# Kernel optimization log

Hardware: AMD Instinct MI355X
Metric: run time of the kernel (lower is better)

## Reference

```python
import jax, jax.numpy as jnp
import numpy as np

EPS = 1e-8

def _unit(v):
    # matches unitization(): v / (||v|| + 1e-8), norm over last (xyz) axis
    return v / (jnp.linalg.norm(v, axis=-1, keepdims=True) + EPS)

def setup_inputs() -> dict:
    key = jax.random.key(0)
    ks = jax.random.split(key, 6)
    B, C, P, S = 16, 76, 1024, 32  # 12 + C_in(=64) channels
    inp = jax.random.normal(ks[0], (B, C, P, S), jnp.float32)
    normal = jax.random.normal(ks[1], (B, P, 3), jnp.float32)
    w1 = jax.random.normal(ks[2], (128, 73), jnp.float32) * 0.1
    b1 = jnp.zeros((128,), jnp.float32)
    w2 = jax.random.normal(ks[3], (128, 128), jnp.float32) * 0.1
    b2 = jnp.zeros((128,), jnp.float32)
    return {"input": inp, "normal": normal, "w1": w1, "b1": b1, "w2": w2, "b2": b2}

def reference(input, normal, w1, b1, w2, b2):
    # channel layout: [0:3]=abs coords, [3:6]=neighbor normals, [6:9]=relative coords,
    # [9:12]=neighbor azimuth dirs, [12:]=input features (C_in=64)
    other_normal = input[:, 3:6]   # (B,3,P,S)
    rel = input[:, 6:9]            # (B,3,P,S)
    other_dir = input[:, 9:12]     # (B,3,P,S)
    feats = input[:, 12:]          # (B,C_in,P,S)

    # azimuth vector: mean of relative coords over neighbors excluding centroid slot
    azi = jnp.mean(rel[:, :, :, 1:], axis=3).transpose(0, 2, 1)  # (B,P,3)

    # PointAlign rotation: local frame with z = unit normal,
    # x = azimuth projected onto tangent plane, y = z x x (row-stacked rotation)
    n = _unit(normal)
    a = _unit(azi)
    xax = _unit(a - jnp.sum(a * n, axis=-1, keepdims=True) * n)
    yax = jnp.cross(n, xax)
    R = jnp.stack([xax, yax, n], axis=2)  # (B,P,3,3)

    def align(v):  # (B,3,P,S) -> (B,3,P,S): rotate each neighbor vector into local frame
        return jnp.einsum('bpij,bjps->bips', R, v)

    azi_u = _unit(azi)                                  # (B,P,3)
    dir_dif = align(azi_u.transpose(0, 2, 1)[:, :, :, None] - other_dir)

    # x[:,0:3] = aligned relative coords, then concat other_normal + dir_difs
    x = jnp.concatenate([align(rel), feats, align(other_normal), dir_dif], axis=1)  # (B,73,P,S)

    # shared MLP: two 1x1 convs + ReLU
    h = jax.nn.relu(jnp.einsum('oc,bcps->bops', w1, x) + b1[None, :, None, None])
    h = jax.nn.relu(jnp.einsum('oc,bcps->bops', w2, h) + b2[None, :, None, None])

    pooled = jnp.max(h, axis=3)  # max_pool2d over nsample -> (B,128,P)
    # not last layer: prepend unit azimuth vector
    return jnp.concatenate([azi_u.transpose(0, 2, 1), pooled], axis=1)  # (B,131,P)
```

## Files before the change

### kernel.cpp

```cpp
#include <hip/hip_runtime.h>
#include <hip/hip_bf16.h>

#define NB 16
#define NP 1024
#define NS 32
#define NC 76
#define XSTR 104
#define HSTR 136
#define TPB 16

typedef __attribute__((ext_vector_type(8))) short bf16x8;
typedef __attribute__((ext_vector_type(4))) float f32x4;

__device__ inline short f2bf(float f) {
  unsigned u = __builtin_bit_cast(unsigned, f);
  u = u + 0x7fffu + ((u >> 16) & 1u);
  return (short)(u >> 16);
}
__device__ inline unsigned cvt_pk_bf16(float lo, float hi) {
  unsigned r;
  asm("v_cvt_pk_bf16_f32 %0, %1, %2" : "=v"(r) : "v"(lo), "v"(hi));
  return r;
}
__device__ inline int swzx(int col, int k) {
  return (col * XSTR + k) ^ (((col >> 4) & 7) << 3);
}
__device__ inline int swzh(int col, int k) {
  return (col * HSTR + k) ^ (((col >> 4) & 7) << 3);
}
__device__ inline float dpp_max16(float v) {
  int x;
  x = __builtin_amdgcn_update_dpp(0, __builtin_bit_cast(int, v), 0xB1, 0xf, 0xf, true);
  v = fmaxf(v, __builtin_bit_cast(float, x));
  x = __builtin_amdgcn_update_dpp(0, __builtin_bit_cast(int, v), 0x4E, 0xf, 0xf, true);
  v = fmaxf(v, __builtin_bit_cast(float, x));
  x = __builtin_amdgcn_update_dpp(0, __builtin_bit_cast(int, v), 0x141, 0xf, 0xf, true);
  v = fmaxf(v, __builtin_bit_cast(float, x));
  x = __builtin_amdgcn_update_dpp(0, __builtin_bit_cast(int, v), 0x140, 0xf, 0xf, true);
  v = fmaxf(v, __builtin_bit_cast(float, x));
  return v;
}

__global__ __launch_bounds__(512, 2)
void mlp_kernel(const float* __restrict__ inp, const float* __restrict__ w1g,
                const float* __restrict__ b1g, const float* __restrict__ w2g,
                const float* __restrict__ b2g, const float* __restrict__ normal,
                float* __restrict__ out) {
  __shared__ short xb[2][128 * XSTR];
  __shared__ short hb[2][128 * HSTR];
  const int tid = threadIdx.x;
  const int lane = tid & 63;
  const int wv = tid >> 6;
  const int wr = wv >> 1;
  const int wc = wv & 1;
  const int l15 = lane & 15;
  const int l4 = lane >> 4;

  const int tile0 = blockIdx.x * TPB;

  const int s4  = tid & 7;
  const int flp = (tid >> 3) & 3;
  const int chq = tid >> 5;
  const int colb = flp*32 + 4*s4;

  bf16x8 w1f[2][3];
#pragma unroll
  for (int mf = 0; mf < 2; ++mf)
#pragma unroll
    for (int ks = 0; ks < 3; ++ks) {
      bf16x8 a;
#pragma unroll
      for (int j = 0; j < 8; ++j) {
        int row = 32*wr + 16*mf + l15;
        int kk = 32*ks + 8*l4 + j;
        float v = 0.f;
        if (kk < 73) {
          int c = (kk < 64) ? (kk + 3) : ((kk < 67) ? (kk - 64) : kk);
          v = w1g[row*73 + c];
        } else if (kk == 73) {
          v = b1g[row];
        }
        a[j] = f2bf(v);
      }
      w1f[mf][ks] = a;
    }
  bf16x8 w2f[2][4];
#pragma unroll
  for (int mf = 0; mf < 2; ++mf)
#pragma unroll
    for (int ks = 0; ks < 4; ++ks) {
      bf16x8 a;
#pragma unroll
      for (int j = 0; j < 8; ++j) {
        int row = 32*wr + 16*mf + l15;
        int kk = 32*ks + 8*l4 + j;
        a[j] = f2bf(w2g[row*128 + kk]);
      }
      w2f[mf][ks] = a;
    }
  float bias2[2][4];
#pragma unroll
  for (int mf = 0; mf < 2; ++mf)
#pragma unroll
    for (int r = 0; r < 4; ++r)
      bias2[mf][r] = b2g[32*wr + 16*mf + 4*l4 + r];

  for (int i = tid; i < 2*128*23; i += 512) {
    int bufi = i / (128*23);
    int r = i - bufi*(128*23);
    int col = r / 23;
    int k = 73 + (r - col*23);
    xb[bufi][swzx(col, k)] = (k == 73) ? (short)0x3F80 : (short)0;
  }

  float4 sf0, sf1, sf2, sf3;
  float sro[9];
  auto stage = [&](int it2) {
    const int tile = tile0 + it2;
    const int bb = tile >> 8;
    const int pb = (tile & 255) * 4;
    const float* base = inp + ((size_t)((bb*NC + 12 + 4*chq)*NP) + pb + flp)*NS + 4*s4;
    sf0 = *(const float4*)(base + 0*(size_t)NP*NS);
    sf1 = *(const float4*)(base + 1*(size_t)NP*NS);
    sf2 = *(const float4*)(base + 2*(size_t)NP*NS);
    sf3 = *(const float4*)(base + 3*(size_t)NP*NS);
    if (tid < 128) {
      const int lp = tid >> 5, s = tid & 31;
      const int p = pb + lp;
#pragma unroll
      for (int i = 0; i < 3; ++i) {
        sro[i]   = inp[(size_t)((bb*NC + 6 + i)*NP + p)*NS + s];
        sro[3+i] = inp[(size_t)((bb*NC + 3 + i)*NP + p)*NS + s];
        sro[6+i] = inp[(size_t)((bb*NC + 9 + i)*NP + p)*NS + s];
      }
    }
  };

  auto fill = [&](int it2, int bufi) {
    const float* f0 = (const float*)&sf0;
    const float* f1 = (const float*)&sf1;
    const float* f2 = (const float*)&sf2;
    const float* f3 = (const float*)&sf3;
#pragma unroll
    for (int j = 0; j < 4; ++j) {
      uint2 pk;
      pk.x = cvt_pk_bf16(f0[j], f1[j]);
      pk.y = cvt_pk_bf16(f2[j], f3[j]);
      *(uint2*)&xb[bufi][swzx(colb + j, 4*chq)] = pk;
    }
    if (tid < 128) {
      const int tile = tile0 + it2;
      const int bb = tile >> 8;
      const int pb = (tile & 255) * 4;
      const int col = tid;
      const int lp = col >> 5, s = col & 31;
      const int p = pb + lp;
      float az[3];
#pragma unroll
      for (int i = 0; i < 3; ++i) {
        float sum = sro[i];
#pragma unroll
        for (int m = 1; m < 32; m <<= 1) sum += __shfl_xor(sum, m);
        float v0 = __shfl(sro[i], lane & 32);
        az[i] = (sum - v0) * (1.f/31.f);
      }
      float nr[3];
#pragma unroll
      for (int i = 0; i < 3; ++i) nr[i] = normal[(size_t)(bb*NP + p)*3 + i];
      float nn = sqrtf(nr[0]*nr[0] + nr[1]*nr[1] + nr[2]*nr[2]) + 1e-8f;
      nr[0] /= nn; nr[1] /= nn; nr[2] /= nn;
      float an = sqrtf(az[0]*az[0] + az[1]*az[1] + az[2]*az[2]) + 1e-8f;
      float au[3] = {az[0]/an, az[1]/an, az[2]/an};
      float d = au[0]*nr[0] + au[1]*nr[1] + au[2]*nr[2];
      float xax[3] = {au[0] - d*nr[0], au[1] - d*nr[1], au[2] - d*nr[2]};
      float xn = sqrtf(xax[0]*xax[0] + xax[1]*xax[1] + xax[2]*xax[2]) + 1e-8f;
      xax[0] /= xn; xax[1] /= xn; xax[2] /= xn;
      float yax[3] = {nr[1]*xax[2] - nr[2]*xax[1],
                      nr[2]*xax[0] - nr[0]*xax[2],
                      nr[0]*xax[1] - nr[1]*xax[0]};
      if (s < 3) {
        float o = (s == 0) ? au[0] : ((s == 1) ? au[1] : au[2]);
        out[(size_t)(bb*131 + s)*NP + p] = o;
      }
      float xv[9];
#pragma unroll
      for (int r = 0; r < 3; ++r) {
        const float* Rr = (r == 0) ? xax : ((r == 1) ? yax : nr);
        xv[r]   = Rr[0]*sro[0] + Rr[1]*sro[1] + Rr[2]*sro[2];
        xv[3+r] = Rr[0]*sro[3] + Rr[1]*sro[4] + Rr[2]*sro[5];
        xv[6+r] = (Rr[0]*au[0] + Rr[1]*au[1] + Rr[2]*au[2])
                - (Rr[0]*sro[6] + Rr[1]*sro[7] + Rr[2]*sro[8]);
      }
      int4 pk;
      pk.x = (int)cvt_pk_bf16(xv[0], xv[1]);
      pk.y = (int)cvt_pk_bf16(xv[2], xv[3]);
      pk.z = (int)cvt_pk_bf16(xv[4], xv[5]);
      pk.w = (int)cvt_pk_bf16(xv[6], xv[7]);
      *(int4*)&xb[bufi][swzx(col, 64)] = pk;
      xb[bufi][swzx(col, 72)] = f2bf(xv[8]);
    }
  };

  f32x4 acc2[2][4];
  auto layer1_h1 = [&](int tt) {
    f32x4 acc1[2][4];
#pragma unroll
    for (int mf = 0; mf < 2; ++mf)
#pragma unroll
      for (int nf = 0; nf < 4; ++nf) acc1[mf][nf] = f32x4{0.f,0.f,0.f,0.f};
    const short* xs = xb[tt & 1];
#pragma unroll
    for (int ks = 0; ks < 3; ++ks) {
      bf16x8 bv[4];
#pragma unroll
      for (int nf = 0; nf < 4; ++nf)
        bv[nf] = *(const bf16x8*)&xs[swzx(64*wc + 16*nf + l15, 32*ks + 8*l4)];
#pragma unroll
      for (int mf = 0; mf < 2; ++mf)
#pragma unroll
        for (int nf = 0; nf < 4; ++nf)
          acc1[mf][nf] = __builtin_amdgcn_mfma_f32_16x16x32_bf16(
              w1f[mf][ks], bv[nf], acc1[mf][nf], 0, 0, 0);
    }
    short* hs = hb[tt & 1];
#pragma unroll
    for (int mf = 0; mf < 2; ++mf)
#pragma unroll
      for (int nf = 0; nf < 4; ++nf) {
        const int col = 64*wc + 16*nf + l15;
        const int row0 = 32*wr + 16*mf + 4*l4;
        uint2 pk;
        pk.x = cvt_pk_bf16(fmaxf(acc1[mf][nf][0], 0.f), fmaxf(acc1[mf][nf][1], 0.f));
        pk.y = cvt_pk_bf16(fmaxf(acc1[mf][nf][2], 0.f), fmaxf(acc1[mf][nf][3], 0.f));
        *(uint2*)&hs[swzh(col, row0)] = pk;
      }
  };
  auto layer2 = [&](int tt) {
#pragma unroll
    for (int mf = 0; mf < 2; ++mf)
#pragma unroll
      for (int nf = 0; nf < 4; ++nf) acc2[mf][nf] = f32x4{0.f,0.f,0.f,0.f};
    const short* hs = hb[tt & 1];
#pragma unroll
    for (int ks = 0; ks < 4; ++ks) {
      bf16x8 bv[4];
#pragma unroll
      for (int nf = 0; nf < 4; ++nf)
        bv[nf] = *(const bf16x8*)&hs[swzh(64*wc + 16*nf + l15, 32*ks + 8*l4)];
#pragma unroll
      for (int mf = 0; mf < 2; ++mf)
#pragma unroll
        for (int nf = 0; nf < 4; ++nf)
          acc2[mf][nf] = __builtin_amdgcn_mfma_f32_16x16x32_bf16(
              w2f[mf][ks], bv[nf], acc2[mf][nf], 0, 0, 0);
    }
  };

  stage(0);
  fill(0, 0);
  stage(1);
  __syncthreads();
  layer1_h1(0);
  fill(1, 1);
  stage(2);
  __syncthreads();

  for (int it = 0; it < TPB; ++it) {
    const int tile = tile0 + it;
    const int bb = tile >> 8;
    const int pb = (tile & 255) * 4;

    layer2(it);

#pragma unroll
    for (int mf = 0; mf < 2; ++mf)
#pragma unroll
      for (int r = 0; r < 4; ++r) {
        float v0 = fmaxf(acc2[mf][0][r], acc2[mf][1][r]);
        float v1 = fmaxf(acc2[mf][2][r], acc2[mf][3][r]);
        v0 = dpp_max16(v0);
        v1 = dpp_max16(v1);
        v0 = fmaxf(v0 + bias2[mf][r], 0.f);
        v1 = fmaxf(v1 + bias2[mf][r], 0.f);
        if (l15 == 0) {
          const int row = 32*wr + 16*mf + 4*l4 + r;
          *(float2*)&out[(size_t)(bb*131 + 3 + row)*NP + pb + 2*wc] = float2{v0, v1};
        }
      }

    if (it + 1 < TPB) layer1_h1(it + 1);
    if (it + 2 < TPB) fill(it + 2, it & 1);
    if (it + 3 < TPB) stage(it + 3);
    if (it + 1 < TPB) __syncthreads();
  }
}

extern "C" void kernel_launch(void* const* d_in, const int* in_sizes, int n_in,
                              void* d_out, int out_size, void* d_ws, size_t ws_size,
                              hipStream_t stream) {
  const float* inp    = (const float*)d_in[0];
  const float* normal = (const float*)d_in[1];
  const float* w1     = (const float*)d_in[2];
  const float* b1     = (const float*)d_in[3];
  const float* w2     = (const float*)d_in[4];
  const float* b2     = (const float*)d_in[5];
  float* out = (float*)d_out;

  mlp_kernel<<<dim3(NB*NP/4/TPB), dim3(512), 0, stream>>>(
      inp, w1, b1, w2, b2, normal, out);
}
```

Before: 60.82 us.

## Give each wave 16 output rows across all columns and swap MFMA operands for pooling

Each wave now owns 16 output channels across all 128 columns instead of a 32x64 tile. Layer 2 swaps the MFMA operands so the neighbor-sample dimension lands in the per-lane accumulator registers, which lets the max-pool run mostly in registers plus two cross-lane shuffles instead of DPP reductions. The change also vectorizes the w2 loads, replaces part of the azimuth shuffle reduction with DPP adds, and hoists the normal loads earlier. Each wave now reads all B fragments from LDS with no reuse across M fragments, which roughly doubles LDS read traffic per MFMA.

```diff
diff --git a/kernel.cpp b/kernel.cpp
--- a/kernel.cpp
+++ b/kernel.cpp
@@ -28,16 +28,16 @@
 __device__ inline int swzh(int col, int k) {
   return (col * HSTR + k) ^ (((col >> 4) & 7) << 3);
 }
-__device__ inline float dpp_max16(float v) {
+__device__ inline float dpp_add16(float v) {
   int x;
   x = __builtin_amdgcn_update_dpp(0, __builtin_bit_cast(int, v), 0xB1, 0xf, 0xf, true);
-  v = fmaxf(v, __builtin_bit_cast(float, x));
+  v += __builtin_bit_cast(float, x);
   x = __builtin_amdgcn_update_dpp(0, __builtin_bit_cast(int, v), 0x4E, 0xf, 0xf, true);
-  v = fmaxf(v, __builtin_bit_cast(float, x));
+  v += __builtin_bit_cast(float, x);
   x = __builtin_amdgcn_update_dpp(0, __builtin_bit_cast(int, v), 0x141, 0xf, 0xf, true);
-  v = fmaxf(v, __builtin_bit_cast(float, x));
+  v += __builtin_bit_cast(float, x);
   x = __builtin_amdgcn_update_dpp(0, __builtin_bit_cast(int, v), 0x140, 0xf, 0xf, true);
-  v = fmaxf(v, __builtin_bit_cast(float, x));
+  v += __builtin_bit_cast(float, x);
   return v;
 }
 
@@ -51,8 +51,6 @@
   const int tid = threadIdx.x;
   const int lane = tid & 63;
   const int wv = tid >> 6;
-  const int wr = wv >> 1;
-  const int wc = wv & 1;
   const int l15 = lane & 15;
   const int l4 = lane >> 4;
 
@@ -63,47 +61,37 @@
   const int chq = tid >> 5;
   const int colb = flp*32 + 4*s4;
 
-  bf16x8 w1f[2][3];
-#pragma unroll
-  for (int mf = 0; mf < 2; ++mf)
-#pragma unroll
-    for (int ks = 0; ks < 3; ++ks) {
-      bf16x8 a;
-#pragma unroll
-      for (int j = 0; j < 8; ++j) {
-        int row = 32*wr + 16*mf + l15;
-        int kk = 32*ks + 8*l4 + j;
-        float v = 0.f;
-        if (kk < 73) {
-          int c = (kk < 64) ? (kk + 3) : ((kk < 67) ? (kk - 64) : kk);
-          v = w1g[row*73 + c];
-        } else if (kk == 73) {
-          v = b1g[row];
-        }
-        a[j] = f2bf(v);
-      }
-      w1f[mf][ks] = a;
-    }
-  bf16x8 w2f[2][4];
-#pragma unroll
-  for (int mf = 0; mf < 2; ++mf)
-#pragma unroll
-    for (int ks = 0; ks < 4; ++ks) {
-      bf16x8 a;
-#pragma unroll
-      for (int j = 0; j < 8; ++j) {
-        int row = 32*wr + 16*mf + l15;
-        int kk = 32*ks + 8*l4 + j;
-        a[j] = f2bf(w2g[row*128 + kk]);
-      }
-      w2f[mf][ks] = a;
-    }
-  float bias2[2][4];
-#pragma unroll
-  for (int mf = 0; mf < 2; ++mf)
-#pragma unroll
-    for (int r = 0; r < 4; ++r)
-      bias2[mf][r] = b2g[32*wr + 16*mf + 4*l4 + r];
+  bf16x8 w1f[3];
+#pragma unroll
+  for (int ks = 0; ks < 3; ++ks) {
+    bf16x8 a;
+#pragma unroll
+    for (int j = 0; j < 8; ++j) {
+      int row = 16*wv + l15;
+      int kk = 32*ks + 8*l4 + j;
+      float v = 0.f;
+      if (kk < 73) {
+        int c = (kk < 64) ? (kk + 3) : ((kk < 67) ? (kk - 64) : kk);
+        v = w1g[row*73 + c];
+      } else if (kk == 73) {
+        v = b1g[row];
+      }
+      a[j] = f2bf(v);
+    }
+    w1f[ks] = a;
+  }
+  bf16x8 w2f[4];
+#pragma unroll
+  for (int ks = 0; ks < 4; ++ks) {
+    const float* wp = w2g + (size_t)(16*wv + l15)*128 + 32*ks + 8*l4;
+    float4 a0 = *(const float4*)wp;
+    float4 a1 = *(const float4*)(wp + 4);
+    bf16x8 a;
+    a[0] = f2bf(a0.x); a[1] = f2bf(a0.y); a[2] = f2bf(a0.z); a[3] = f2bf(a0.w);
+    a[4] = f2bf(a1.x); a[5] = f2bf(a1.y); a[6] = f2bf(a1.z); a[7] = f2bf(a1.w);
+    w2f[ks] = a;
+  }
+  const float bias2s = b2g[16*wv + l15];
 
   for (int i = tid; i < 2*128*23; i += 512) {
     int bufi = i / (128*23);
@@ -137,6 +125,15 @@
   };
 
   auto fill = [&](int it2, int bufi) {
+    const int tile = tile0 + it2;
+    const int bb = tile >> 8;
+    const int pb = (tile & 255) * 4;
+    float nr[3];
+    if (tid < 128) {
+      const int p = pb + (tid >> 5);
+#pragma unroll
+      for (int i = 0; i < 3; ++i) nr[i] = normal[(size_t)(bb*NP + p)*3 + i];
+    }
     const float* f0 = (const float*)&sf0;
     const float* f1 = (const float*)&sf1;
     const float* f2 = (const float*)&sf2;
@@ -149,24 +146,17 @@
       *(uint2*)&xb[bufi][swzx(colb + j, 4*chq)] = pk;
     }
     if (tid < 128) {
-      const int tile = tile0 + it2;
-      const int bb = tile >> 8;
-      const int pb = (tile & 255) * 4;
       const int col = tid;
-      const int lp = col >> 5, s = col & 31;
-      const int p = pb + lp;
+      const int s = col & 31;
+      const int p = pb + (col >> 5);
       float az[3];
 #pragma unroll
       for (int i = 0; i < 3; ++i) {
-        float sum = sro[i];
-#pragma unroll
-        for (int m = 1; m < 32; m <<= 1) sum += __shfl_xor(sum, m);
+        float sum = dpp_add16(sro[i]);
+        sum += __shfl_xor(sum, 16);
         float v0 = __shfl(sro[i], lane & 32);
         az[i] = (sum - v0) * (1.f/31.f);
       }
-      float nr[3];
-#pragma unroll
-      for (int i = 0; i < 3; ++i) nr[i] = normal[(size_t)(bb*NP + p)*3 + i];
       float nn = sqrtf(nr[0]*nr[0] + nr[1]*nr[1] + nr[2]*nr[2]) + 1e-8f;
       nr[0] /= nn; nr[1] /= nn; nr[2] /= nn;
       float an = sqrtf(az[0]*az[0] + az[1]*az[1] + az[2]*az[2]) + 1e-8f;
@@ -201,58 +191,48 @@
     }
   };
 
-  f32x4 acc2[2][4];
+  f32x4 acc2[8];
   auto layer1_h1 = [&](int tt) {
-    f32x4 acc1[2][4];
-#pragma unroll
-    for (int mf = 0; mf < 2; ++mf)
-#pragma unroll
-      for (int nf = 0; nf < 4; ++nf) acc1[mf][nf] = f32x4{0.f,0.f,0.f,0.f};
+    f32x4 acc1[8];
+#pragma unroll
+    for (int nf = 0; nf < 8; ++nf) acc1[nf] = f32x4{0.f,0.f,0.f,0.f};
     const short* xs = xb[tt & 1];
 #pragma unroll
     for (int ks = 0; ks < 3; ++ks) {
-      bf16x8 bv[4];
-#pragma unroll
-      for (int nf = 0; nf < 4; ++nf)
-        bv[nf] = *(const bf16x8*)&xs[swzx(64*wc + 16*nf + l15, 32*ks + 8*l4)];
-#pragma unroll
-      for (int mf = 0; mf < 2; ++mf)
-#pragma unroll
-        for (int nf = 0; nf < 4; ++nf)
-          acc1[mf][nf] = __builtin_amdgcn_mfma_f32_16x16x32_bf16(
-              w1f[mf][ks], bv[nf], acc1[mf][nf], 0, 0, 0);
+      bf16x8 bv[8];
+#pragma unroll
+      for (int nf = 0; nf < 8; ++nf)
+        bv[nf] = *(const bf16x8*)&xs[swzx(16*nf + l15, 32*ks + 8*l4)];
+#pragma unroll
+      for (int nf = 0; nf < 8; ++nf)
+        acc1[nf] = __builtin_amdgcn_mfma_f32_16x16x32_bf16(
+            w1f[ks], bv[nf], acc1[nf], 0, 0, 0);
     }
     short* hs = hb[tt & 1];
 #pragma unroll
-    for (int mf = 0; mf < 2; ++mf)
-#pragma unroll
-      for (int nf = 0; nf < 4; ++nf) {
-        const int col = 64*wc + 16*nf + l15;
-        const int row0 = 32*wr + 16*mf + 4*l4;
-        uint2 pk;
-        pk.x = cvt_pk_bf16(fmaxf(acc1[mf][nf][0], 0.f), fmaxf(acc1[mf][nf][1], 0.f));
-        pk.y = cvt_pk_bf16(fmaxf(acc1[mf][nf][2], 0.f), fmaxf(acc1[mf][nf][3], 0.f));
-        *(uint2*)&hs[swzh(col, row0)] = pk;
-      }
+    for (int nf = 0; nf < 8; ++nf) {
+      const int col = 16*nf + l15;
+      const int row0 = 16*wv + 4*l4;
+      uint2 pk;
+      pk.x = cvt_pk_bf16(fmaxf(acc1[nf][0], 0.f), fmaxf(acc1[nf][1], 0.f));
+      pk.y = cvt_pk_bf16(fmaxf(acc1[nf][2], 0.f), fmaxf(acc1[nf][3], 0.f));
+      *(uint2*)&hs[swzh(col, row0)] = pk;
+    }
   };
   auto layer2 = [&](int tt) {
 #pragma unroll
-    for (int mf = 0; mf < 2; ++mf)
-#pragma unroll
-      for (int nf = 0; nf < 4; ++nf) acc2[mf][nf] = f32x4{0.f,0.f,0.f,0.f};
+    for (int nf = 0; nf < 8; ++nf) acc2[nf] = f32x4{0.f,0.f,0.f,0.f};
     const short* hs = hb[tt & 1];
 #pragma unroll
     for (int ks = 0; ks < 4; ++ks) {
-      bf16x8 bv[4];
-#pragma unroll
-      for (int nf = 0; nf < 4; ++nf)
-        bv[nf] = *(const bf16x8*)&hs[swzh(64*wc + 16*nf + l15, 32*ks + 8*l4)];
-#pragma unroll
-      for (int mf = 0; mf < 2; ++mf)
-#pragma unroll
-        for (int nf = 0; nf < 4; ++nf)
-          acc2[mf][nf] = __builtin_amdgcn_mfma_f32_16x16x32_bf16(
-              w2f[mf][ks], bv[nf], acc2[mf][nf], 0, 0, 0);
+      bf16x8 bv[8];
+#pragma unroll
+      for (int nf = 0; nf < 8; ++nf)
+        bv[nf] = *(const bf16x8*)&hs[swzh(16*nf + l15, 32*ks + 8*l4)];
+#pragma unroll
+      for (int nf = 0; nf < 8; ++nf)
+        acc2[nf] = __builtin_amdgcn_mfma_f32_16x16x32_bf16(
+            bv[nf], w2f[ks], acc2[nf], 0, 0, 0);
     }
   };
 
@@ -272,21 +252,21 @@
 
     layer2(it);
 
-#pragma unroll
-    for (int mf = 0; mf < 2; ++mf)
-#pragma unroll
-      for (int r = 0; r < 4; ++r) {
-        float v0 = fmaxf(acc2[mf][0][r], acc2[mf][1][r]);
-        float v1 = fmaxf(acc2[mf][2][r], acc2[mf][3][r]);
-        v0 = dpp_max16(v0);
-        v1 = dpp_max16(v1);
-        v0 = fmaxf(v0 + bias2[mf][r], 0.f);
-        v1 = fmaxf(v1 + bias2[mf][r], 0.f);
-        if (l15 == 0) {
-          const int row = 32*wr + 16*mf + 4*l4 + r;
-          *(float2*)&out[(size_t)(bb*131 + 3 + row)*NP + pb + 2*wc] = float2{v0, v1};
-        }
-      }
+    float m[8];
+#pragma unroll
+    for (int nf = 0; nf < 8; ++nf)
+      m[nf] = fmaxf(fmaxf(acc2[nf][0], acc2[nf][1]),
+                    fmaxf(acc2[nf][2], acc2[nf][3]));
+    float vp[4];
+#pragma unroll
+    for (int p = 0; p < 4; ++p) {
+      float v = fmaxf(m[2*p], m[2*p+1]);
+      v = fmaxf(v, __shfl_xor(v, 16));
+      v = fmaxf(v, __shfl_xor(v, 32));
+      vp[p] = fmaxf(v + bias2s, 0.f);
+    }
+    float vsel = (l4 == 0) ? vp[0] : (l4 == 1) ? vp[1] : (l4 == 2) ? vp[2] : vp[3];
+    out[(size_t)(bb*131 + 3 + 16*wv + l15)*NP + pb + l4] = vsel;
 
     if (it + 1 < TPB) layer1_h1(it + 1);
     if (it + 2 < TPB) fill(it + 2, it & 1);
```

After: 61.04 us. No clear change (+0.4%).
